# Kernel optimization log

Measured on AMD Instinct MI355X. Metric: run time of the kernel, lower is better.

## Reference

```python
import jax, jax.numpy as jnp
import numpy as np

K = 3          # hypergraph neighbors (hardcoded self.kn = 3)
H = 3          # attention heads (hardcoded num_heads=3)
QKD = 32       # qkv_dim
BN_EPS = 1e-5


def _pe(channels, num_frames):
    # Ter_Embed: sinusoidal over frame index, constant across joints -> (1,C,T,1)
    pos = jnp.arange(num_frames, dtype=jnp.float32)
    div = jnp.exp(jnp.arange(0, channels, 2, dtype=jnp.float32) * (-np.log(10000.0) / channels))
    ang = pos[:, None] * div[None, :]                      # (T, C/2)
    pe = jnp.zeros((num_frames, channels), jnp.float32)
    pe = pe.at[:, 0::2].set(jnp.sin(ang)).at[:, 1::2].set(jnp.cos(ang))
    return pe.T[None, :, :, None]                          # (1,C,T,1)


def _bn(x, g, b):
    # training-mode BatchNorm2d over (N,T,V) per channel
    mu = x.mean(axis=(0, 2, 3), keepdims=True)
    var = x.var(axis=(0, 2, 3), keepdims=True)
    return (x - mu) * jax.lax.rsqrt(var + BN_EPS) * g[None, :, None, None] + b[None, :, None, None]


def setup_inputs() -> dict:
    key = jax.random.key(0)
    ks = jax.random.split(key, 16)
    N, C, T, V = 8, 128, 64, 204
    s = 0.05
    inp = {
        'x': jax.random.normal(ks[0], (N, C, T, V), jnp.float32),
        # Transform.conv1: Conv1d(k, k*k, C, groups=k) -> weight (k*k, 1, C)
        'trans_w': jax.random.normal(ks[1], (K * K, C), jnp.float32) * s,
        'trans_b': jax.random.normal(ks[2], (K * K,), jnp.float32) * s,
        # VertexConv.convK1: Conv1d(k, 1, 1)
        'convk_w': jax.random.normal(ks[3], (K,), jnp.float32) * s,
        'convk_b': jax.random.normal(ks[4], (1,), jnp.float32) * s,
        # to_qkvs: Conv2d(C, 2*H*QKD, 1)
        'qkv_w': jax.random.normal(ks[5], (2 * H * QKD, C), jnp.float32) * s,
        'qkv_b': jax.random.normal(ks[6], (2 * H * QKD,), jnp.float32) * s,
        'alphas': jnp.ones((1, H, 1, 1), jnp.float32),
        'att1s': jnp.broadcast_to(jnp.eye(T, dtype=jnp.float32), (1, H, T, T)) + 0.0,
        # out_nets: Conv2d(H*C, C, (1,1)) + BN
        'out_w': jax.random.normal(ks[7], (C, H * C), jnp.float32) * s,
        'out_b': jax.random.normal(ks[8], (C,), jnp.float32) * s,
        'out_g': jnp.ones((C,), jnp.float32) + jax.random.normal(ks[9], (C,), jnp.float32) * 0.01,
        'out_beta': jax.random.normal(ks[10], (C,), jnp.float32) * 0.01,
        # ff_net: Conv2d(C, C, 1) + BN
        'ff_w': jax.random.normal(ks[11], (C, C), jnp.float32) * s,
        'ff_b': jax.random.normal(ks[12], (C,), jnp.float32) * s,
        'ff_g': jnp.ones((C,), jnp.float32) + jax.random.normal(ks[13], (C,), jnp.float32) * 0.01,
        'ff_beta': jax.random.normal(ks[14], (C,), jnp.float32) * 0.01,
    }
    return inp


def reference(x, trans_w, trans_b, convk_w, convk_b, qkv_w, qkv_b, alphas, att1s,
              out_w, out_b, out_g, out_beta, ff_w, ff_b, ff_g, ff_beta):
    N, C, T, V = x.shape
    orign = x
    # ---------- hypergraph_knn (ssa) ----------
    # cos_dis: F.normalize over last dim (V) then contract c,t -> (N,V,V)
    nrm = jnp.linalg.norm(x, axis=-1, keepdims=True)
    xn = x / jnp.maximum(nrm, 1e-12)
    dis = jnp.einsum('nctu,nctv->nuv', xn, xn)
    _, idx = jax.lax.top_k(dis, K)                                   # (N,V,K)
    # gather neighbor feats: feats[n,c,t,v,k] = x[n,c,t,idx[n,v,k]]
    feats = jnp.take_along_axis(x[:, :, :, None, :], idx[:, None, None, :, :], axis=4)  # (N,C,T,V,K)
    # Transform: grouped Conv1d over C, group g -> K outputs
    m = feats.mean(axis=2).transpose(0, 2, 3, 1)                     # (N,V,K,C)
    mult = jnp.einsum('nvgc,gpc->nvgp', m, trans_w.reshape(K, K, C)) + trans_b.reshape(K, K)
    mult = jax.nn.softmax(mult, axis=-1)                             # (N,V,K,K)
    transformed = jnp.einsum('nctvk,nvkp->nctvp', feats, mult)
    # convK1 pools K -> 1
    pooled = jnp.einsum('nctvk,k->nctv', transformed, convk_w) + convk_b[0]
    x = jax.nn.relu(pooled + orign)
    # ---------- TTA_Block_att ----------
    xs = x + _pe(C, T)
    qkv = jnp.einsum('oc,nctv->notv', qkv_w, xs) + qkv_b[None, :, None, None]
    qkv = qkv.reshape(N, 2 * H, QKD, T, V)
    q, k = qkv[:, :H], qkv[:, H:]
    att = jnp.tanh(jnp.einsum('nhctv,nhcqv->nhtq', q, k) / (QKD * V)) * alphas + att1s  # (N,H,T,T)
    xs2 = jnp.einsum('nctv,nstq->nscqv', x, att).reshape(N, H * C, T, V)
    out = jnp.einsum('os,nstv->notv', out_w, xs2) + out_b[None, :, None, None]
    out = _bn(out, out_g, out_beta)
    xs3 = jax.nn.leaky_relu(out + x, 0.1)                            # ress is identity (in==out)
    ff = jnp.einsum('oc,nctv->notv', ff_w, xs3) + ff_b[None, :, None, None]
    ff = _bn(ff, ff_g, ff_beta)
    return jax.nn.leaky_relu(ff + x, 0.1)
```

## Files before the change

### kernel.cpp

```cpp
#include <hip/hip_runtime.h>
#include <math.h>

#define N_ 8
#define C_ 128
#define T_ 64
#define V_ 204
#define H_ 3
#define QKD_ 32
#define O2_ 192
#define TV_ 13056
#define CT_ 8192
#define TT_ 4096
#define VV_ 41616
#define NCTV_ 13369344ull
#define DSPLIT_ 32
#define ZR_ 208
#define NBLK_ 1632

typedef __attribute__((ext_vector_type(8))) short short8v;
typedef __attribute__((ext_vector_type(4))) float f32x4;

__device__ inline unsigned short bf16rnd(float f) {
  union { float f; unsigned u; } x; x.f = f;
  return (unsigned short)((x.u + 0x7FFFu + ((x.u >> 16) & 1u)) >> 16);
}
__device__ inline float bf2f(unsigned short u) {
  union { unsigned u; float f; } x; x.u = ((unsigned)u) << 16;
  return x.f;
}

__global__ void k_wprep(const float* __restrict__ qw, const float* __restrict__ ow,
                        const float* __restrict__ fw, unsigned short* __restrict__ wb) {
  int g = blockIdx.x * 256 + threadIdx.x;
  if (g >= 704 * 16) return;
  int row = g >> 4, ch = g & 15;
  const float* src;
  if (row < 192) src = qw + row * 128;
  else if (row < 576) { int r = row - 192; src = ow + (r & 127) * 384 + (r >> 7) * 128; }
  else src = fw + (row - 576) * 128;
  f32x4 a = *(const f32x4*)(src + ch * 8);
  f32x4 b = *(const f32x4*)(src + ch * 8 + 4);
  unsigned short buf[8];
  buf[0] = bf16rnd(a.x); buf[1] = bf16rnd(a.y); buf[2] = bf16rnd(a.z); buf[3] = bf16rnd(a.w);
  buf[4] = bf16rnd(b.x); buf[5] = bf16rnd(b.y); buf[6] = bf16rnd(b.z); buf[7] = bf16rnd(b.w);
  *(uint4*)(wb + (size_t)row * 128 + ch * 8) = *(const uint4*)buf;
}

__global__ void k_qkvpe(const float* __restrict__ qw, const float* __restrict__ qb,
                        float* __restrict__ qpe) {
  __shared__ float pes[C_ * T_];
  int tid = threadIdx.x;
  for (int i = tid; i < C_ * T_; i += 256) {
    int t = i & 63, c = i >> 6;
    int j = c >> 1;
    float dv = expf((2.0f * j) * (-logf(10000.0f) / (float)C_));
    float ang = (float)t * dv;
    pes[i] = (c & 1) ? cosf(ang) : sinf(ang);
  }
  __syncthreads();
  int g = blockIdx.x * 256 + tid;
  int t = g & 63, m = g >> 6;
  float a = 0.f;
  for (int c = 0; c < C_; ++c) a += qw[m * C_ + c] * pes[c * T_ + t];
  qpe[g] = a + qb[m];
}

__global__ void k_scale(const float* __restrict__ x, float* __restrict__ s) {
  int gid = blockIdx.x * blockDim.x + threadIdx.x;
  int w = gid >> 6, lane = gid & 63;
  if (w >= N_ * CT_) return;
  const f32x4* row = (const f32x4*)(x + (size_t)w * V_);
  float a = 0.f;
  for (int v4 = lane; v4 < 51; v4 += 64) {
    f32x4 t = row[v4];
    a += t.x * t.x + t.y * t.y + t.z * t.z + t.w * t.w;
  }
#pragma unroll
  for (int off = 32; off >= 1; off >>= 1) a += __shfl_down(a, off, 64);
  if (lane == 0) {
    float d = fmaxf(sqrtf(a), 1e-12f);
    s[w] = 1.0f / (d * d);
  }
}

__global__ __launch_bounds__(256) void k_zprep(const float* __restrict__ x,
                                               const float* __restrict__ s,
                                               unsigned short* __restrict__ zhi,
                                               unsigned short* __restrict__ zlo,
                                               float* __restrict__ cm) {
  int kt = blockIdx.x, ut = blockIdx.y, n = blockIdx.z;
  int k0 = kt * 64, u0 = ut * 64;
  __shared__ float Ts[64][65];
  __shared__ float sq[64];
  int tid = threadIdx.x;
  int uu = tid & 63, kk = tid >> 6;
  int u = u0 + uu;
  bool uok = u < V_;
  const float* xb = x + (size_t)n * CT_ * V_;
#pragma unroll
  for (int it = 0; it < 16; ++it) {
    int kr = kk + it * 4;
    Ts[kr][uu] = uok ? xb[(size_t)(k0 + kr) * V_ + u] : 0.f;
  }
  if (tid < 64) sq[tid] = sqrtf(s[(size_t)n * CT_ + k0 + tid]);
  __syncthreads();
  if (tid < 64 && uok) {
    float a = 0.f;
    for (int t = 0; t < 64; ++t) a += Ts[t][tid];
    cm[((size_t)n * C_ + kt) * V_ + u] = a * (1.0f / 64.0f);
  }
#pragma unroll
  for (int it = 0; it < 4; ++it) {
    int sl = tid + it * 256;
    int u_l = sl & 63, oct = (sl >> 6) & 7, half = sl >> 9;
    int ug = u0 + u_l;
    if (ug >= ZR_) continue;
    unsigned short buf[8];
    if (ug < V_) {
#pragma unroll
      for (int j = 0; j < 8; ++j) {
        float z = Ts[oct * 8 + j][u_l] * sq[oct * 8 + j];
        unsigned short h = bf16rnd(z);
        buf[j] = half ? bf16rnd(z - bf2f(h)) : h;
      }
    } else {
#pragma unroll
      for (int j = 0; j < 8; ++j) buf[j] = 0;
    }
    unsigned short* dst = (half ? zlo : zhi) +
                          (((size_t)n * 1024 + kt * 8 + oct) * ZR_ + ug) * 8;
    *(uint4*)dst = *(const uint4*)buf;
  }
}

__global__ __launch_bounds__(256) void k_dism(const unsigned short* __restrict__ zhi,
                                              const unsigned short* __restrict__ zlo,
                                              float* __restrict__ pdis) {
  int q = blockIdx.x, sp = blockIdx.y, n = blockIdx.z;
  int bu = (q == 2) ? 1 : 0, bv = (q == 0) ? 0 : 1;
  int u0 = bu * 128, v0 = bv * 128;
  bool dg = (bu == bv);
  __shared__ unsigned short As[8 * 128 * 8];
  __shared__ unsigned short Bs[8 * 128 * 8];
  int tid = threadIdx.x, lane = tid & 63, wid = tid >> 6;
  int lr = lane & 15, lg = lane >> 4;
  f32x4 acc[2][8];
#pragma unroll
  for (int mi = 0; mi < 2; ++mi)
#pragma unroll
    for (int li = 0; li < 8; ++li) acc[mi][li] = (f32x4){0.f, 0.f, 0.f, 0.f};
  const int KCH = CT_ / DSPLIT_;
  int kbase = sp * KCH, kend = kbase + KCH;
  for (int kk = kbase; kk < kend; kk += 32) {
    int koct = kk >> 3;
    __syncthreads();
#pragma unroll
    for (int it = 0; it < 4; ++it) {
      int sl = tid + it * 256;
      int row = sl & 127, hs = sl >> 7;
      int slot = hs & 3, half = hs >> 2;
      const unsigned short* src = half ? zlo : zhi;
      size_t ob = ((size_t)n * 1024 + koct + slot) * ZR_;
      int ra = u0 + row; ra = ra > 207 ? 207 : ra;
      *(uint4*)&As[(hs * 128 + row) * 8] = *(const uint4*)(src + (ob + ra) * 8);
      if (!dg) {
        int rb = v0 + row; rb = rb > 207 ? 207 : rb;
        *(uint4*)&Bs[(hs * 128 + row) * 8] = *(const uint4*)(src + (ob + rb) * 8);
      }
    }
    __syncthreads();
    const unsigned short* Bp = dg ? As : Bs;
    short8v ah[2], al[2];
#pragma unroll
    for (int mi = 0; mi < 2; ++mi) {
      int r = wid * 32 + mi * 16 + lr;
      ah[mi] = *(const short8v*)&As[(lg * 128 + r) * 8];
      al[mi] = *(const short8v*)&As[((4 + lg) * 128 + r) * 8];
    }
#pragma unroll
    for (int li = 0; li < 8; ++li) {
      int rv = li * 16 + lr;
      short8v bh = *(const short8v*)&Bp[(lg * 128 + rv) * 8];
      short8v bl = *(const short8v*)&Bp[((4 + lg) * 128 + rv) * 8];
#pragma unroll
      for (int mi = 0; mi < 2; ++mi) {
        acc[mi][li] = __builtin_amdgcn_mfma_f32_16x16x32_bf16(ah[mi], bh, acc[mi][li], 0, 0, 0);
        acc[mi][li] = __builtin_amdgcn_mfma_f32_16x16x32_bf16(ah[mi], bl, acc[mi][li], 0, 0, 0);
        acc[mi][li] = __builtin_amdgcn_mfma_f32_16x16x32_bf16(al[mi], bh, acc[mi][li], 0, 0, 0);
      }
    }
  }
  float* pb = pdis + ((size_t)sp * N_ + n) * VV_;
#pragma unroll
  for (int mi = 0; mi < 2; ++mi) {
#pragma unroll
    for (int li = 0; li < 8; ++li) {
      int v = v0 + li * 16 + lr;
      if (v >= V_) continue;
#pragma unroll
      for (int rr = 0; rr < 4; ++rr) {
        int u = u0 + wid * 32 + mi * 16 + lg * 4 + rr;
        if (u >= V_) continue;
        float val = acc[mi][li][rr];
        pb[(size_t)u * V_ + v] = val;
        if (!dg) pb[(size_t)v * V_ + u] = val;
      }
    }
  }
}

__global__ void k_topk2(const float* __restrict__ pdis, int* __restrict__ idx) {
  int r = blockIdx.x;
  int n = r / V_, u = r - n * V_;
  int lane = threadIdx.x;
  float m0 = -INFINITY, m1 = -INFINITY, m2 = -INFINITY;
  int i0 = 0x7fffffff, i1 = 0x7fffffff, i2 = 0x7fffffff;
#pragma unroll
  for (int g = 0; g < 4; ++g) {
    int v = g * 64 + lane;
    if (v >= V_) break;
    float a = 0.f;
#pragma unroll
    for (int sp = 0; sp < DSPLIT_; ++sp)
      a += pdis[((size_t)sp * N_ + n) * VV_ + (size_t)u * V_ + v];
    if (a > m0 || (a == m0 && v < i0)) {
      m2 = m1; i2 = i1; m1 = m0; i1 = i0; m0 = a; i0 = v;
    } else if (a > m1 || (a == m1 && v < i1)) {
      m2 = m1; i2 = i1; m1 = a; i1 = v;
    } else if (a > m2 || (a == m2 && v < i2)) {
      m2 = a; i2 = v;
    }
  }
#pragma unroll
  for (int msk = 1; msk < 64; msk <<= 1) {
    float o0 = __shfl_xor(m0, msk, 64), o1 = __shfl_xor(m1, msk, 64),
          o2 = __shfl_xor(m2, msk, 64);
    int p0 = __shfl_xor(i0, msk, 64), p1 = __shfl_xor(i1, msk, 64),
        p2 = __shfl_xor(i2, msk, 64);
    float ov[3] = {o0, o1, o2};
    int op[3] = {p0, p1, p2};
#pragma unroll
    for (int e = 0; e < 3; ++e) {
      float a = ov[e]; int v = op[e];
      if (a > m0 || (a == m0 && v < i0)) {
        m2 = m1; i2 = i1; m1 = m0; i1 = i0; m0 = a; i0 = v;
      } else if (a > m1 || (a == m1 && v < i1)) {
        m2 = m1; i2 = i1; m1 = a; i1 = v;
      } else if (a > m2 || (a == m2 && v < i2)) {
        m2 = a; i2 = v;
      }
    }
  }
  if (lane == 0) {
    idx[r * 3 + 0] = i0; idx[r * 3 + 1] = i1; idx[r * 3 + 2] = i2;
  }
}

__global__ void k_w2(const float* __restrict__ cm, const int* __restrict__ idx,
                     const float* __restrict__ tw, const float* __restrict__ tb,
                     const float* __restrict__ ckw, float* __restrict__ w2) {
  int r = blockIdx.x;
  int n = r / V_;
  int lane = threadIdx.x;
  __shared__ float mv[3][C_];
  const int* ib = idx + r * 3;
  int j0 = ib[0], j1 = ib[1], j2 = ib[2];
  const float* cmn = cm + (size_t)n * C_ * V_;
  for (int c = lane; c < C_; c += 64) {
    mv[0][c] = cmn[c * V_ + j0];
    mv[1][c] = cmn[c * V_ + j1];
    mv[2][c] = cmn[c * V_ + j2];
  }
  __syncthreads();
  float p[9];
#pragma unroll
  for (int gp = 0; gp < 9; ++gp) p[gp] = 0.f;
  for (int c = lane; c < C_; c += 64) {
#pragma unroll
    for (int g = 0; g < 3; ++g) {
      float m = mv[g][c];
#pragma unroll
      for (int pp = 0; pp < 3; ++pp) p[g * 3 + pp] += m * tw[(g * 3 + pp) * C_ + c];
    }
  }
#pragma unroll
  for (int off = 32; off >= 1; off >>= 1) {
#pragma unroll
    for (int gp = 0; gp < 9; ++gp) p[gp] += __shfl_down(p[gp], off, 64);
  }
  if (lane == 0) {
    float c0 = ckw[0], c1 = ckw[1], c2 = ckw[2];
#pragma unroll
    for (int g = 0; g < 3; ++g) {
      float m0 = p[g * 3 + 0] + tb[g * 3 + 0];
      float m1 = p[g * 3 + 1] + tb[g * 3 + 1];
      float m2 = p[g * 3 + 2] + tb[g * 3 + 2];
      float mx = fmaxf(m0, fmaxf(m1, m2));
      float e0 = expf(m0 - mx), e1 = expf(m1 - mx), e2 = expf(m2 - mx);
      float inv = 1.0f / (e0 + e1 + e2);
      w2[r * 3 + g] = (e0 * c0 + e1 * c1 + e2 * c2) * inv;
    }
  }
}

__global__ __launch_bounds__(256) void k_x1p(const float* __restrict__ x,
                                             const int* __restrict__ idx,
                                             const float* __restrict__ w2,
                                             const float* __restrict__ ckb,
                                             unsigned short* __restrict__ x1pb) {
  int t = blockIdx.x, ct = blockIdx.y, n = blockIdx.z;
  int c0 = ct * 32;
  __shared__ float Ts[32][209];
  __shared__ int iw[V_ * 3];
  __shared__ float ww[V_ * 3];
  int tid = threadIdx.x;
  const float* xb = x + ((size_t)n * C_ + c0) * TV_ + t * V_;
  for (int i = tid; i < 32 * V_; i += 256) {
    int c = i / V_, v = i - c * V_;
    Ts[c][v] = xb[(size_t)c * TV_ + v];
  }
  for (int i = tid; i < V_ * 3; i += 256) {
    iw[i] = idx[(size_t)n * V_ * 3 + i];
    ww[i] = w2[(size_t)n * V_ * 3 + i];
  }
  __syncthreads();
  float cb = ckb[0];
  for (int i = tid; i < 32 * V_; i += 256) {
    int v = i >> 5, cl = i & 31;
    int b = v * 3;
    float pooled = Ts[cl][iw[b]] * ww[b] + Ts[cl][iw[b + 1]] * ww[b + 1] +
                   Ts[cl][iw[b + 2]] * ww[b + 2] + cb;
    float val = fmaxf(pooled + Ts[cl][v], 0.f);
    x1pb[((size_t)(n * V_ + v) * T_ + t) * C_ + c0 + cl] = bf16rnd(val);
  }
}

template <int MCH, int OBF, int STATS>
__global__ __launch_bounds__(256) void k_gmm2(const unsigned short* __restrict__ Wb,
                                              const unsigned short* __restrict__ Xp,
                                              const float* __restrict__ addv,
                                              void* __restrict__ Yv,
                                              float* __restrict__ part) {
  int l0 = blockIdx.x * 128, n = blockIdx.z;
  __shared__ unsigned short Xs[128 * 136];
  __shared__ unsigned short Ys[64 * 128];
  int tid = threadIdx.x, lane = tid & 63, wid = tid >> 6;
  int wm = wid >> 1, wl = wid & 1;
  int lr = lane & 15, lg = lane >> 4;
  const unsigned short* xb = Xp + ((size_t)n * TV_ + l0) * 128;
#pragma unroll
  for (int it = 0; it < 8; ++it) {
    int g = tid + it * 256;
    int row = g >> 4, ch = g & 15;
    *(uint4*)&Xs[row * 136 + ch * 8] = *(const uint4*)(xb + (size_t)row * 128 + ch * 8);
  }
  __syncthreads();
  for (int mc = 0; mc < MCH; ++mc) {
    short8v a[2][4];
#pragma unroll
    for (int mi = 0; mi < 2; ++mi) {
      int m = mc * 64 + wm * 32 + mi * 16 + lr;
#pragma unroll
      for (int ks = 0; ks < 4; ++ks)
        a[mi][ks] = *(const short8v*)(Wb + (size_t)m * 128 + ks * 32 + lg * 8);
    }
    f32x4 acc[2][4];
#pragma unroll
    for (int mi = 0; mi < 2; ++mi)
#pragma unroll
      for (int li = 0; li < 4; ++li) acc[mi][li] = (f32x4){0.f, 0.f, 0.f, 0.f};
#pragma unroll
    for (int ks = 0; ks < 4; ++ks) {
#pragma unroll
      for (int li = 0; li < 4; ++li) {
        short8v b = *(const short8v*)&Xs[(wl * 64 + li * 16 + lr) * 136 + ks * 32 + lg * 8];
#pragma unroll
        for (int mi = 0; mi < 2; ++mi)
          acc[mi][li] = __builtin_amdgcn_mfma_f32_16x16x32_bf16(a[mi][ks], b, acc[mi][li], 0, 0, 0);
      }
    }
    if (OBF) {
      __syncthreads();
#pragma unroll
      for (int mi = 0; mi < 2; ++mi)
#pragma unroll
        for (int li = 0; li < 4; ++li) {
          int lloc = wl * 64 + li * 16 + lr;
          int tt = (l0 + lloc) & 63;
#pragma unroll
          for (int r = 0; r < 4; ++r) {
            int mloc = wm * 32 + mi * 16 + lg * 4 + r;
            float val = acc[mi][li][r] + addv[(mc * 64 + mloc) * 64 + tt];
            Ys[mloc * 128 + lloc] = bf16rnd(val);
          }
        }
      __syncthreads();
      unsigned short* Yh = (unsigned short*)Yv;
#pragma unroll
      for (int it = 0; it < 4; ++it) {
        int g = tid + it * 256;
        int row = g >> 4, ch = g & 15;
        *(uint4*)(Yh + ((size_t)n * O2_ + mc * 64 + row) * TV_ + l0 + ch * 8) =
            *(const uint4*)&Ys[row * 128 + ch * 8];
      }
    } else {
      unsigned short* Yh = (unsigned short*)Yv;
      float st1[2][4] = {}, st2[2][4] = {};
#pragma unroll
      for (int mi = 0; mi < 2; ++mi)
#pragma unroll
        for (int li = 0; li < 4; ++li) {
          int lp = l0 + wl * 64 + li * 16 + lr;
          int m = mc * 64 + wm * 32 + mi * 16 + lg * 4;
          unsigned short b4[4];
#pragma unroll
          for (int r = 0; r < 4; ++r) {
            float val = acc[mi][li][r] + addv[m + r];
            if (STATS) { st1[mi][r] += val; st2[mi][r] += val * val; }
            b4[r] = bf16rnd(val);
          }
          *(uint2*)(Yh + ((size_t)n * TV_ + lp) * 128 + m) = *(const uint2*)b4;
        }
      if (STATS) {
        int blk2 = ((n * gridDim.x + blockIdx.x) * 2 + wl) * 256;
#pragma unroll
        for (int mi = 0; mi < 2; ++mi)
#pragma unroll
          for (int r = 0; r < 4; ++r) {
            float a1 = st1[mi][r], a2 = st2[mi][r];
            a1 += __shfl_xor(a1, 1, 64); a2 += __shfl_xor(a2, 1, 64);
            a1 += __shfl_xor(a1, 2, 64); a2 += __shfl_xor(a2, 2, 64);
            a1 += __shfl_xor(a1, 4, 64); a2 += __shfl_xor(a2, 4, 64);
            a1 += __shfl_xor(a1, 8, 64); a2 += __shfl_xor(a2, 8, 64);
            if (lr == 0) {
              int m = mc * 64 + wm * 32 + mi * 16 + lg * 4 + r;
              part[blk2 + m] = a1;
              part[blk2 + 128 + m] = a2;
            }
          }
      }
    }
  }
}

__global__ __launch_bounds__(256) void k_att(const unsigned short* __restrict__ qkv,
                                             float* __restrict__ attp) {
  int cp = blockIdx.x, h = blockIdx.y, n = blockIdx.z;
  __shared__ float Qs[102][68], Ks[102][68];
  int tid = threadIdx.x;
  int ty = tid >> 4, tx = tid & 15;
  float acc[4][4] = {};
  for (int cc = 0; cc < 2; ++cc) {
    int c = cp * 2 + cc;
    const unsigned short* qb = qkv + ((size_t)n * O2_ + h * QKD_ + c) * TV_;
    const unsigned short* kb = qkv + ((size_t)n * O2_ + H_ * QKD_ + h * QKD_ + c) * TV_;
    for (int vh = 0; vh < 2; ++vh) {
      for (int g = tid; g < 816; g += 256) {
        int v = g >> 3, t0 = (g & 7) * 8;
        uint4 qv = *(const uint4*)(qb + vh * 6528 + g * 8);
        uint4 kv = *(const uint4*)(kb + vh * 6528 + g * 8);
        const unsigned short* qs = (const unsigned short*)&qv;
        const unsigned short* ks2 = (const unsigned short*)&kv;
#pragma unroll
        for (int j = 0; j < 8; ++j) {
          Qs[v][t0 + j] = bf2f(qs[j]);
          Ks[v][t0 + j] = bf2f(ks2[j]);
        }
      }
      __syncthreads();
      for (int vv = 0; vv < 102; ++vv) {
        f32x4 qa = *(const f32x4*)&Qs[vv][ty * 4];
        f32x4 ka = *(const f32x4*)&Ks[vv][tx * 4];
#pragma unroll
        for (int i = 0; i < 4; ++i)
#pragma unroll
          for (int j = 0; j < 4; ++j) acc[i][j] += qa[i] * ka[j];
      }
      __syncthreads();
    }
  }
  float* ar = attp + (((size_t)cp * N_ + n) * H_ + h) * TT_;
#pragma unroll
  for (int i = 0; i < 4; ++i)
#pragma unroll
    for (int j = 0; j < 4; ++j)
      ar[(ty * 4 + i) * T_ + tx * 4 + j] = acc[i][j];
}

__global__ void k_attfin(const float* __restrict__ attp, const float* __restrict__ alphas,
                         const float* __restrict__ att1s, unsigned short* __restrict__ attT) {
  int i = blockIdx.x * blockDim.x + threadIdx.x;
  if (i >= N_ * H_ * TT_) return;
  int tt = i % TT_;
  int h = (i / TT_) % H_;
  int n = i / (H_ * TT_);
  float raw = 0.f;
#pragma unroll
  for (int cp = 0; cp < 16; ++cp)
    raw += attp[(((size_t)cp * N_ + n) * H_ + h) * TT_ + tt];
  int t = tt >> 6, q = tt & 63;
  float v = tanhf(raw * (1.0f / 6528.0f)) * alphas[h] + att1s[h * TT_ + tt];
  attT[(size_t)(n * 64 + q) * 192 + h * 64 + t] = bf16rnd(v);
}

__global__ __launch_bounds__(256) void k_fcomb(const unsigned short* __restrict__ x1pb,
                                               const unsigned short* __restrict__ w3b,
                                               const unsigned short* __restrict__ attT,
                                               const float* __restrict__ outb,
                                               unsigned short* __restrict__ preb,
                                               float* __restrict__ part) {
  int v = blockIdx.x, n = blockIdx.z;
  __shared__ unsigned short Yv[2][128 * 68];
  int tid = threadIdx.x, lane = tid & 63, wid = tid >> 6;
  int lr = lane & 15, lg = lane >> 4;
  const unsigned short* xb = x1pb + ((size_t)(n * V_ + v) * T_) * 128;
  short8v bx[4][4];
#pragma unroll
  for (int ks = 0; ks < 4; ++ks)
#pragma unroll
    for (int li = 0; li < 4; ++li)
      bx[ks][li] = *(const short8v*)(xb + (size_t)(li * 16 + lr) * 128 + ks * 32 + lg * 8);
  f32x4 acc2[4][2];
#pragma unroll
  for (int mq = 0; mq < 4; ++mq)
#pragma unroll
    for (int oi = 0; oi < 2; ++oi) acc2[mq][oi] = (f32x4){0.f, 0.f, 0.f, 0.f};
  const unsigned short* ab = attT + (size_t)n * 64 * 192;
  for (int h = 0; h < H_; ++h) {
    unsigned short* Yc = Yv[h & 1];
    short8v a1[2][4];
#pragma unroll
    for (int mi = 0; mi < 2; ++mi) {
      int m = wid * 32 + mi * 16 + lr;
#pragma unroll
      for (int ks = 0; ks < 4; ++ks)
        a1[mi][ks] = *(const short8v*)(w3b + ((size_t)(h * 128 + m)) * 128 + ks * 32 + lg * 8);
    }
    f32x4 acc1[2][4];
#pragma unroll
    for (int mi = 0; mi < 2; ++mi)
#pragma unroll
      for (int li = 0; li < 4; ++li) acc1[mi][li] = (f32x4){0.f, 0.f, 0.f, 0.f};
#pragma unroll
    for (int ks = 0; ks < 4; ++ks)
#pragma unroll
      for (int li = 0; li < 4; ++li)
#pragma unroll
        for (int mi = 0; mi < 2; ++mi)
          acc1[mi][li] = __builtin_amdgcn_mfma_f32_16x16x32_bf16(a1[mi][ks], bx[ks][li],
                                                                 acc1[mi][li], 0, 0, 0);
#pragma unroll
    for (int mi = 0; mi < 2; ++mi)
#pragma unroll
      for (int li = 0; li < 4; ++li) {
        int t = li * 16 + lr;
#pragma unroll
        for (int r = 0; r < 4; ++r) {
          int o = wid * 32 + mi * 16 + lg * 4 + r;
          Yc[o * 68 + t] = bf16rnd(acc1[mi][li][r]);
        }
      }
    __syncthreads();
#pragma unroll
    for (int ks2 = 0; ks2 < 2; ++ks2) {
      short8v bY[2];
#pragma unroll
      for (int oi = 0; oi < 2; ++oi)
        bY[oi] = *(const short8v*)&Yc[(wid * 32 + oi * 16 + lr) * 68 + ks2 * 32 + lg * 8];
#pragma unroll
      for (int mq = 0; mq < 4; ++mq) {
        short8v a2 = *(const short8v*)(ab + (size_t)(mq * 16 + lr) * 192 + h * 64 + ks2 * 32 + lg * 8);
#pragma unroll
        for (int oi = 0; oi < 2; ++oi)
          acc2[mq][oi] = __builtin_amdgcn_mfma_f32_16x16x32_bf16(a2, bY[oi], acc2[mq][oi], 0, 0, 0);
      }
    }
  }
  unsigned short* Ys2 = Yv[1];
  float s1[2] = {0.f, 0.f}, s2[2] = {0.f, 0.f};
#pragma unroll
  for (int mq = 0; mq < 4; ++mq)
#pragma unroll
    for (int oi = 0; oi < 2; ++oi) {
      int o = wid * 32 + oi * 16 + lr;
      float bo = outb[o];
#pragma unroll
      for (int r = 0; r < 4; ++r) {
        int q = mq * 16 + lg * 4 + r;
        float val = acc2[mq][oi][r] + bo;
        s1[oi] += val; s2[oi] += val * val;
        Ys2[q * 136 + o] = bf16rnd(val);
      }
    }
  int blk = (n * V_ + v) * 256;
#pragma unroll
  for (int oi = 0; oi < 2; ++oi) {
    float a1 = s1[oi], a2 = s2[oi];
    a1 += __shfl_xor(a1, 16, 64); a2 += __shfl_xor(a2, 16, 64);
    a1 += __shfl_xor(a1, 32, 64); a2 += __shfl_xor(a2, 32, 64);
    if ((lane & 48) == 0) {
      int o = wid * 32 + oi * 16 + lr;
      part[blk + o] = a1;
      part[blk + 128 + o] = a2;
    }
  }
  __syncthreads();
  unsigned short* ob2 = preb + ((size_t)(n * V_ + v) * T_) * 128;
#pragma unroll
  for (int it = 0; it < 4; ++it) {
    int g = tid + it * 256;
    int row = g >> 4, ch = g & 15;
    *(uint4*)(ob2 + (size_t)row * 128 + ch * 8) = *(const uint4*)&Ys2[row * 136 + ch * 8];
  }
}

__global__ void k_bnab(const float* __restrict__ part, const float* __restrict__ g,
                       const float* __restrict__ beta, float* __restrict__ ab) {
  int c = blockIdx.x;
  int tid = threadIdx.x;
  float s1 = 0.f, s2 = 0.f;
  for (int b = tid; b < NBLK_; b += 256) {
    s1 += part[b * 256 + c];
    s2 += part[b * 256 + 128 + c];
  }
  __shared__ float r1[256], r2[256];
  r1[tid] = s1; r2[tid] = s2;
  __syncthreads();
  for (int off = 128; off >= 1; off >>= 1) {
    if (tid < off) { r1[tid] += r1[tid + off]; r2[tid] += r2[tid + off]; }
    __syncthreads();
  }
  if (tid == 0) {
    const float cnt = (float)(N_ * TV_);
    float mu = r1[0] / cnt;
    float rstd = rsqrtf(r2[0] / cnt - mu * mu + 1e-5f);
    float a = rstd * g[c];
    ab[c] = a;
    ab[128 + c] = beta[c] - mu * a;
  }
}

__global__ void k_bnxt(const unsigned short* __restrict__ preb,
                       const unsigned short* __restrict__ x1pb,
                       const float* __restrict__ ab, unsigned short* __restrict__ xt) {
  __shared__ float sa[128], sb[128];
  int tid = threadIdx.x;
  if (tid < 128) { sa[tid] = ab[tid]; sb[tid] = ab[128 + tid]; }
  __syncthreads();
  const unsigned NU = (unsigned)(NCTV_ / 8);
  const uint4* p4 = (const uint4*)preb;
  const uint4* r4 = (const uint4*)x1pb;
  for (unsigned u = blockIdx.x * 256u + tid; u < NU; u += gridDim.x * 256u) {
    int c8 = (u & 15) * 8;
    uint4 pv = p4[u], rv = r4[u];
    const unsigned short* ps = (const unsigned short*)&pv;
    const unsigned short* rs = (const unsigned short*)&rv;
    unsigned short buf[8];
#pragma unroll
    for (int j = 0; j < 8; ++j) {
      float t = bf2f(ps[j]) * sa[c8 + j] + sb[c8 + j] + bf2f(rs[j]);
      buf[j] = bf16rnd(t > 0.f ? t : 0.1f * t);
    }
    *(uint4*)(xt + (size_t)u * 8) = *(const uint4*)buf;
  }
}

__global__ __launch_bounds__(256) void k_bnfinal(const unsigned short* __restrict__ preb,
                                                 const unsigned short* __restrict__ x1pb,
                                                 const float* __restrict__ ab,
                                                 float* __restrict__ dout) {
  int ct = blockIdx.x, t = blockIdx.y, n = blockIdx.z;
  int c0 = ct * 32;
  __shared__ float Tf[V_][33];
  __shared__ float sa[32], sb[32];
  int tid = threadIdx.x;
  if (tid < 32) { sa[tid] = ab[c0 + tid]; sb[tid] = ab[128 + c0 + tid]; }
  __syncthreads();
  for (int i = tid; i < V_ * 4; i += 256) {
    int v = i >> 2, ch = i & 3;
    size_t a = ((size_t)(n * V_ + v) * T_ + t) * 128 + c0 + ch * 8;
    uint4 pv = *(const uint4*)(preb + a);
    uint4 rv = *(const uint4*)(x1pb + a);
    const unsigned short* ps = (const unsigned short*)&pv;
    const unsigned short* rs = (const unsigned short*)&rv;
#pragma unroll
    for (int j = 0; j < 8; ++j) {
      int cl = ch * 8 + j;
      float val = bf2f(ps[j]) * sa[cl] + sb[cl] + bf2f(rs[j]);
      Tf[v][cl] = val > 0.f ? val : 0.1f * val;
    }
  }
  __syncthreads();
  for (int i = tid; i < 32 * V_; i += 256) {
    int cl = i / V_, v = i - cl * V_;
    dout[((size_t)(n * C_ + c0 + cl) * T_ + t) * V_ + v] = Tf[v][cl];
  }
}

extern "C" void kernel_launch(void* const* d_in, const int* in_sizes, int n_in,
                              void* d_out, int out_size, void* d_ws, size_t ws_size,
                              hipStream_t stream) {
  (void)in_sizes; (void)n_in; (void)out_size; (void)ws_size;
  const float* x        = (const float*)d_in[0];
  const float* trans_w  = (const float*)d_in[1];
  const float* trans_b  = (const float*)d_in[2];
  const float* convk_w  = (const float*)d_in[3];
  const float* convk_b  = (const float*)d_in[4];
  const float* qkv_w    = (const float*)d_in[5];
  const float* qkv_b    = (const float*)d_in[6];
  const float* alphas   = (const float*)d_in[7];
  const float* att1s    = (const float*)d_in[8];
  const float* out_w    = (const float*)d_in[9];
  const float* out_b    = (const float*)d_in[10];
  const float* out_g    = (const float*)d_in[11];
  const float* out_beta = (const float*)d_in[12];
  const float* ff_w     = (const float*)d_in[13];
  const float* ff_b     = (const float*)d_in[14];
  const float* ff_g     = (const float*)d_in[15];
  const float* ff_beta  = (const float*)d_in[16];

  float* ws = (float*)d_ws;
  size_t off = 0;
  float* gq = ws + off; off += (size_t)N_ * O2_ * TV_ / 2 + NCTV_ / 2;
  float* pdis = gq;
  unsigned short* qkvb = (unsigned short*)gq;
  unsigned short* preb = (unsigned short*)(gq + (size_t)N_ * O2_ * TV_ / 2);
  float* sbuf = ws + off; off += (size_t)N_ * CT_;
  int*   idx  = (int*)(ws + off); off += (size_t)N_ * V_ * 3 + 4;
  float* cm   = ws + off; off += (size_t)N_ * C_ * V_;
  float* w2   = ws + off; off += (size_t)N_ * V_ * 3 + 4;
  float* attp = ws + off; off += (size_t)16 * N_ * H_ * TT_;
  unsigned short* attT = (unsigned short*)(ws + off); off += (size_t)N_ * 64 * 192 / 2;
  float* part = ws + off; off += (size_t)NBLK_ * 256;
  float* ab   = ws + off; off += 512;
  float* qpe  = ws + off; off += (size_t)O2_ * T_;
  unsigned short* wb = (unsigned short*)(ws + off); off += 704 * 128 / 2;
  const size_t ZEL = (size_t)N_ * 1024 * ZR_ * 8;
  unsigned short* zhi = (unsigned short*)(ws + off);
  unsigned short* zlo = zhi + ZEL;
  off += ZEL;
  unsigned short* x1pb  = zhi;
  unsigned short* xs3pb = zlo;
  float* dout = (float*)d_out;

  k_wprep<<<44, 256, 0, stream>>>(qkv_w, out_w, ff_w, wb);
  k_qkvpe<<<48, 256, 0, stream>>>(qkv_w, qkv_b, qpe);
  k_scale<<<(N_ * CT_ * 64) / 256, 256, 0, stream>>>(x, sbuf);
  k_zprep<<<dim3(128, 4, N_), 256, 0, stream>>>(x, sbuf, zhi, zlo, cm);
  k_dism<<<dim3(3, DSPLIT_, N_), 256, 0, stream>>>(zhi, zlo, pdis);
  k_topk2<<<N_ * V_, 64, 0, stream>>>(pdis, idx);
  k_w2<<<N_ * V_, 64, 0, stream>>>(cm, idx, trans_w, trans_b, convk_w, w2);
  k_x1p<<<dim3(64, 4, N_), 256, 0, stream>>>(x, idx, w2, convk_b, x1pb);

  k_gmm2<3, 1, 0><<<dim3(102, 1, N_), 256, 0, stream>>>(wb, x1pb, qpe, qkvb, nullptr);
  k_att<<<dim3(16, H_, N_), 256, 0, stream>>>(qkvb, attp);
  k_attfin<<<384, 256, 0, stream>>>(attp, alphas, att1s, attT);

  k_fcomb<<<dim3(204, 1, N_), 256, 0, stream>>>(x1pb, wb + 192 * 128, attT, out_b, preb, part);

  k_bnab<<<128, 256, 0, stream>>>(part, out_g, out_beta, ab);
  k_bnxt<<<2048, 256, 0, stream>>>(preb, x1pb, ab, xs3pb);

  k_gmm2<2, 0, 1><<<dim3(102, 1, N_), 256, 0, stream>>>(wb + 576 * 128, xs3pb, ff_b, preb, part);
  k_bnab<<<128, 256, 0, stream>>>(part, ff_g, ff_beta, ab + 256);
  k_bnfinal<<<dim3(4, 64, N_), 256, 0, stream>>>(preb, x1pb, ab + 256, dout);
}
```

Measured before the change: 323.6 us.

## Repartition fcomb per-wave over time rows and use direct global-to-LDS loads

In the fused attention/out-projection kernel, each wave now owns 16 time rows and all 128 output channels, loading weights directly from global per MFMA. This replaces the previous output-channel split and shrinks the LDS buffer to a single Y tile. BN partial sums are written per wave, so the partial buffer and the k_bnab reduction count grow fourfold. Separately, the dismat kernel stages tiles through global_load_lds instead of register round-trips, which reduces VGPR traffic but changes the LDS write layout to linear slot order.

```diff
diff --git a/kernel.cpp b/kernel.cpp
--- a/kernel.cpp
+++ b/kernel.cpp
@@ -15,7 +15,6 @@
 #define NCTV_ 13369344ull
 #define DSPLIT_ 32
 #define ZR_ 208
-#define NBLK_ 1632
 
 typedef __attribute__((ext_vector_type(8))) short short8v;
 typedef __attribute__((ext_vector_type(4))) float f32x4;
@@ -27,6 +26,10 @@
 __device__ inline float bf2f(unsigned short u) {
   union { unsigned u; float f; } x; x.u = ((unsigned)u) << 16;
   return x.f;
+}
+__device__ inline void gload_lds16(const unsigned short* g, unsigned short* l) {
+  __builtin_amdgcn_global_load_lds((const __attribute__((address_space(1))) void*)g,
+                                   (__attribute__((address_space(3))) void*)l, 16, 0, 0);
 }
 
 __global__ void k_wprep(const float* __restrict__ qw, const float* __restrict__ ow,
@@ -162,10 +165,10 @@
       const unsigned short* src = half ? zlo : zhi;
       size_t ob = ((size_t)n * 1024 + koct + slot) * ZR_;
       int ra = u0 + row; ra = ra > 207 ? 207 : ra;
-      *(uint4*)&As[(hs * 128 + row) * 8] = *(const uint4*)(src + (ob + ra) * 8);
+      gload_lds16(src + (ob + ra) * 8, &As[sl * 8]);
       if (!dg) {
         int rb = v0 + row; rb = rb > 207 ? 207 : rb;
-        *(uint4*)&Bs[(hs * 128 + row) * 8] = *(const uint4*)(src + (ob + rb) * 8);
+        gload_lds16(src + (ob + rb) * 8, &Bs[sl * 8]);
       }
     }
     __syncthreads();
@@ -510,98 +513,76 @@
                                                unsigned short* __restrict__ preb,
                                                float* __restrict__ part) {
   int v = blockIdx.x, n = blockIdx.z;
-  __shared__ unsigned short Yv[2][128 * 68];
+  __shared__ unsigned short Yv[128 * 68];
   int tid = threadIdx.x, lane = tid & 63, wid = tid >> 6;
   int lr = lane & 15, lg = lane >> 4;
   const unsigned short* xb = x1pb + ((size_t)(n * V_ + v) * T_) * 128;
-  short8v bx[4][4];
+  short8v bx[4];
 #pragma unroll
   for (int ks = 0; ks < 4; ++ks)
-#pragma unroll
-    for (int li = 0; li < 4; ++li)
-      bx[ks][li] = *(const short8v*)(xb + (size_t)(li * 16 + lr) * 128 + ks * 32 + lg * 8);
-  f32x4 acc2[4][2];
-#pragma unroll
-  for (int mq = 0; mq < 4; ++mq)
-#pragma unroll
-    for (int oi = 0; oi < 2; ++oi) acc2[mq][oi] = (f32x4){0.f, 0.f, 0.f, 0.f};
+    bx[ks] = *(const short8v*)(xb + (size_t)(wid * 16 + lr) * 128 + ks * 32 + lg * 8);
+  f32x4 acc2[8];
+#pragma unroll
+  for (int oi = 0; oi < 8; ++oi) acc2[oi] = (f32x4){0.f, 0.f, 0.f, 0.f};
   const unsigned short* ab = attT + (size_t)n * 64 * 192;
+#pragma unroll
   for (int h = 0; h < H_; ++h) {
-    unsigned short* Yc = Yv[h & 1];
-    short8v a1[2][4];
-#pragma unroll
-    for (int mi = 0; mi < 2; ++mi) {
-      int m = wid * 32 + mi * 16 + lr;
-#pragma unroll
-      for (int ks = 0; ks < 4; ++ks)
-        a1[mi][ks] = *(const short8v*)(w3b + ((size_t)(h * 128 + m)) * 128 + ks * 32 + lg * 8);
-    }
-    f32x4 acc1[2][4];
-#pragma unroll
-    for (int mi = 0; mi < 2; ++mi)
-#pragma unroll
-      for (int li = 0; li < 4; ++li) acc1[mi][li] = (f32x4){0.f, 0.f, 0.f, 0.f};
-#pragma unroll
-    for (int ks = 0; ks < 4; ++ks)
-#pragma unroll
-      for (int li = 0; li < 4; ++li)
-#pragma unroll
-        for (int mi = 0; mi < 2; ++mi)
-          acc1[mi][li] = __builtin_amdgcn_mfma_f32_16x16x32_bf16(a1[mi][ks], bx[ks][li],
-                                                                 acc1[mi][li], 0, 0, 0);
-#pragma unroll
-    for (int mi = 0; mi < 2; ++mi)
-#pragma unroll
-      for (int li = 0; li < 4; ++li) {
-        int t = li * 16 + lr;
-#pragma unroll
-        for (int r = 0; r < 4; ++r) {
-          int o = wid * 32 + mi * 16 + lg * 4 + r;
-          Yc[o * 68 + t] = bf16rnd(acc1[mi][li][r]);
-        }
-      }
+    f32x4 acc1[8];
+#pragma unroll
+    for (int mi = 0; mi < 8; ++mi) {
+      acc1[mi] = (f32x4){0.f, 0.f, 0.f, 0.f};
+      const unsigned short* wr = w3b + ((size_t)(h * 128 + mi * 16 + lr)) * 128;
+#pragma unroll
+      for (int ks = 0; ks < 4; ++ks) {
+        short8v a1 = *(const short8v*)(wr + ks * 32 + lg * 8);
+        acc1[mi] = __builtin_amdgcn_mfma_f32_16x16x32_bf16(a1, bx[ks], acc1[mi], 0, 0, 0);
+      }
+    }
     __syncthreads();
+    int t = wid * 16 + lr;
+#pragma unroll
+    for (int mi = 0; mi < 8; ++mi)
+#pragma unroll
+      for (int r = 0; r < 4; ++r) {
+        int o = mi * 16 + lg * 4 + r;
+        Yv[o * 68 + t] = bf16rnd(acc1[mi][r]);
+      }
+    __syncthreads();
 #pragma unroll
     for (int ks2 = 0; ks2 < 2; ++ks2) {
-      short8v bY[2];
-#pragma unroll
-      for (int oi = 0; oi < 2; ++oi)
-        bY[oi] = *(const short8v*)&Yc[(wid * 32 + oi * 16 + lr) * 68 + ks2 * 32 + lg * 8];
-#pragma unroll
-      for (int mq = 0; mq < 4; ++mq) {
-        short8v a2 = *(const short8v*)(ab + (size_t)(mq * 16 + lr) * 192 + h * 64 + ks2 * 32 + lg * 8);
-#pragma unroll
-        for (int oi = 0; oi < 2; ++oi)
-          acc2[mq][oi] = __builtin_amdgcn_mfma_f32_16x16x32_bf16(a2, bY[oi], acc2[mq][oi], 0, 0, 0);
-      }
-    }
-  }
-  unsigned short* Ys2 = Yv[1];
-  float s1[2] = {0.f, 0.f}, s2[2] = {0.f, 0.f};
-#pragma unroll
-  for (int mq = 0; mq < 4; ++mq)
-#pragma unroll
-    for (int oi = 0; oi < 2; ++oi) {
-      int o = wid * 32 + oi * 16 + lr;
-      float bo = outb[o];
-#pragma unroll
-      for (int r = 0; r < 4; ++r) {
-        int q = mq * 16 + lg * 4 + r;
-        float val = acc2[mq][oi][r] + bo;
-        s1[oi] += val; s2[oi] += val * val;
-        Ys2[q * 136 + o] = bf16rnd(val);
-      }
-    }
-  int blk = (n * V_ + v) * 256;
-#pragma unroll
-  for (int oi = 0; oi < 2; ++oi) {
-    float a1 = s1[oi], a2 = s2[oi];
-    a1 += __shfl_xor(a1, 16, 64); a2 += __shfl_xor(a2, 16, 64);
-    a1 += __shfl_xor(a1, 32, 64); a2 += __shfl_xor(a2, 32, 64);
-    if ((lane & 48) == 0) {
-      int o = wid * 32 + oi * 16 + lr;
-      part[blk + o] = a1;
-      part[blk + 128 + o] = a2;
+      short8v a2 = *(const short8v*)(ab + (size_t)(wid * 16 + lr) * 192 + h * 64 + ks2 * 32 + lg * 8);
+#pragma unroll
+      for (int oi = 0; oi < 8; ++oi) {
+        short8v bY = *(const short8v*)&Yv[(oi * 16 + lr) * 68 + ks2 * 32 + lg * 8];
+        acc2[oi] = __builtin_amdgcn_mfma_f32_16x16x32_bf16(a2, bY, acc2[oi], 0, 0, 0);
+      }
+    }
+  }
+  __syncthreads();
+  float s1o[8], s2o[8];
+#pragma unroll
+  for (int oi = 0; oi < 8; ++oi) {
+    int o = oi * 16 + lr;
+    float bo = outb[o];
+    float s1 = 0.f, s2 = 0.f;
+#pragma unroll
+    for (int r = 0; r < 4; ++r) {
+      int qq = wid * 16 + lg * 4 + r;
+      float val = acc2[oi][r] + bo;
+      s1 += val; s2 += val * val;
+      Yv[qq * 136 + o] = bf16rnd(val);
+    }
+    s1o[oi] = s1; s2o[oi] = s2;
+  }
+  int blk = ((n * V_ + v) * 4 + wid) * 256;
+#pragma unroll
+  for (int oi = 0; oi < 8; ++oi) {
+    float a1 = s1o[oi], a2v = s2o[oi];
+    a1 += __shfl_xor(a1, 16, 64); a2v += __shfl_xor(a2v, 16, 64);
+    a1 += __shfl_xor(a1, 32, 64); a2v += __shfl_xor(a2v, 32, 64);
+    if (lg == 0) {
+      part[blk + oi * 16 + lr] = a1;
+      part[blk + 128 + oi * 16 + lr] = a2v;
     }
   }
   __syncthreads();
@@ -610,16 +591,17 @@
   for (int it = 0; it < 4; ++it) {
     int g = tid + it * 256;
     int row = g >> 4, ch = g & 15;
-    *(uint4*)(ob2 + (size_t)row * 128 + ch * 8) = *(const uint4*)&Ys2[row * 136 + ch * 8];
-  }
-}
-
-__global__ void k_bnab(const float* __restrict__ part, const float* __restrict__ g,
-                       const float* __restrict__ beta, float* __restrict__ ab) {
+    *(uint4*)(ob2 + (size_t)row * 128 + ch * 8) = *(const uint4*)&Yv[row * 136 + ch * 8];
+  }
+}
+
+__global__ void k_bnab(const float* __restrict__ part, int count,
+                       const float* __restrict__ g, const float* __restrict__ beta,
+                       float* __restrict__ ab) {
   int c = blockIdx.x;
   int tid = threadIdx.x;
   float s1 = 0.f, s2 = 0.f;
-  for (int b = tid; b < NBLK_; b += 256) {
+  for (int b = tid; b < count; b += 256) {
     s1 += part[b * 256 + c];
     s2 += part[b * 256 + 128 + c];
   }
@@ -731,7 +713,7 @@
   float* w2   = ws + off; off += (size_t)N_ * V_ * 3 + 4;
   float* attp = ws + off; off += (size_t)16 * N_ * H_ * TT_;
   unsigned short* attT = (unsigned short*)(ws + off); off += (size_t)N_ * 64 * 192 / 2;
-  float* part = ws + off; off += (size_t)NBLK_ * 256;
+  float* part = ws + off; off += (size_t)6528 * 256;
   float* ab   = ws + off; off += 512;
   float* qpe  = ws + off; off += (size_t)O2_ * T_;
   unsigned short* wb = (unsigned short*)(ws + off); off += 704 * 128 / 2;
@@ -758,10 +740,10 @@
 
   k_fcomb<<<dim3(204, 1, N_), 256, 0, stream>>>(x1pb, wb + 192 * 128, attT, out_b, preb, part);
 
-  k_bnab<<<128, 256, 0, stream>>>(part, out_g, out_beta, ab);
+  k_bnab<<<128, 256, 0, stream>>>(part, 6528, out_g, out_beta, ab);
   k_bnxt<<<2048, 256, 0, stream>>>(preb, x1pb, ab, xs3pb);
 
   k_gmm2<2, 0, 1><<<dim3(102, 1, N_), 256, 0, stream>>>(wb + 576 * 128, xs3pb, ff_b, preb, part);
-  k_bnab<<<128, 256, 0, stream>>>(part, ff_g, ff_beta, ab + 256);
+  k_bnab<<<128, 256, 0, stream>>>(part, 1632, ff_g, ff_beta, ab + 256);
   k_bnfinal<<<dim3(4, 64, N_), 256, 0, stream>>>(preb, x1pb, ab + 256, dout);
 }
```

Measured after the change: 367.0 us. 1.13x slower.

## Move attention scores to MFMA with position-major qkv layout and async LDS loads

Applied to the files above, without the earlier changes.

The QKV GEMM now writes its output position-major (row per (v,t), 192 channels) instead of channel-major through an LDS transpose. The scalar-FMA attention-score kernel is replaced by one that reads q/k fragments straight from global memory into bf16 MFMA ops, splitting V across waves and reducing in LDS. The distance kernel's tile loads switch to direct global-to-LDS loads, and an extra barrier is added in the fused combine kernel. The aim is to cut the scalar FLOP cost of the attention scores and the LDS staging overhead, at the risk of strided 16-byte global reads in the new attention kernel.

```diff
diff --git a/kernel.cpp b/kernel.cpp
--- a/kernel.cpp
+++ b/kernel.cpp
@@ -28,6 +28,10 @@
   union { unsigned u; float f; } x; x.u = ((unsigned)u) << 16;
   return x.f;
 }
+__device__ inline void gload_lds16(const unsigned short* g, unsigned short* l) {
+  __builtin_amdgcn_global_load_lds((const __attribute__((address_space(1))) void*)g,
+                                   (__attribute__((address_space(3))) void*)l, 16, 0, 0);
+}
 
 __global__ void k_wprep(const float* __restrict__ qw, const float* __restrict__ ow,
                         const float* __restrict__ fw, unsigned short* __restrict__ wb) {
@@ -162,10 +166,10 @@
       const unsigned short* src = half ? zlo : zhi;
       size_t ob = ((size_t)n * 1024 + koct + slot) * ZR_;
       int ra = u0 + row; ra = ra > 207 ? 207 : ra;
-      *(uint4*)&As[(hs * 128 + row) * 8] = *(const uint4*)(src + (ob + ra) * 8);
+      gload_lds16(src + (ob + ra) * 8, &As[sl * 8]);
       if (!dg) {
         int rb = v0 + row; rb = rb > 207 ? 207 : rb;
-        *(uint4*)&Bs[(hs * 128 + row) * 8] = *(const uint4*)(src + (ob + rb) * 8);
+        gload_lds16(src + (ob + rb) * 8, &Bs[sl * 8]);
       }
     }
     __syncthreads();
@@ -335,15 +339,15 @@
   }
 }
 
-template <int MCH, int OBF, int STATS>
+template <int MCH, int PEB, int STATS>
 __global__ __launch_bounds__(256) void k_gmm2(const unsigned short* __restrict__ Wb,
                                               const unsigned short* __restrict__ Xp,
                                               const float* __restrict__ addv,
-                                              void* __restrict__ Yv,
+                                              unsigned short* __restrict__ Yh,
                                               float* __restrict__ part) {
+  const int MS = MCH * 64;
   int l0 = blockIdx.x * 128, n = blockIdx.z;
   __shared__ unsigned short Xs[128 * 136];
-  __shared__ unsigned short Ys[64 * 128];
   int tid = threadIdx.x, lane = tid & 63, wid = tid >> 6;
   int wm = wid >> 1, wl = wid & 1;
   int lr = lane & 15, lg = lane >> 4;
@@ -379,112 +383,98 @@
           acc[mi][li] = __builtin_amdgcn_mfma_f32_16x16x32_bf16(a[mi][ks], b, acc[mi][li], 0, 0, 0);
       }
     }
-    if (OBF) {
-      __syncthreads();
+    float st1[2][4] = {}, st2[2][4] = {};
+#pragma unroll
+    for (int mi = 0; mi < 2; ++mi)
+#pragma unroll
+      for (int li = 0; li < 4; ++li) {
+        int lp = l0 + wl * 64 + li * 16 + lr;
+        int m = mc * 64 + wm * 32 + mi * 16 + lg * 4;
+        unsigned short b4[4];
+#pragma unroll
+        for (int r = 0; r < 4; ++r) {
+          float val = acc[mi][li][r] +
+                      (PEB ? addv[(m + r) * 64 + (lp & 63)] : addv[m + r]);
+          if (STATS) { st1[mi][r] += val; st2[mi][r] += val * val; }
+          b4[r] = bf16rnd(val);
+        }
+        *(uint2*)(Yh + ((size_t)n * TV_ + lp) * MS + m) = *(const uint2*)b4;
+      }
+    if (STATS) {
+      int blk2 = ((n * gridDim.x + blockIdx.x) * 2 + wl) * 256;
 #pragma unroll
       for (int mi = 0; mi < 2; ++mi)
 #pragma unroll
-        for (int li = 0; li < 4; ++li) {
-          int lloc = wl * 64 + li * 16 + lr;
-          int tt = (l0 + lloc) & 63;
-#pragma unroll
-          for (int r = 0; r < 4; ++r) {
-            int mloc = wm * 32 + mi * 16 + lg * 4 + r;
-            float val = acc[mi][li][r] + addv[(mc * 64 + mloc) * 64 + tt];
-            Ys[mloc * 128 + lloc] = bf16rnd(val);
+        for (int r = 0; r < 4; ++r) {
+          float a1 = st1[mi][r], a2 = st2[mi][r];
+          a1 += __shfl_xor(a1, 1, 64); a2 += __shfl_xor(a2, 1, 64);
+          a1 += __shfl_xor(a1, 2, 64); a2 += __shfl_xor(a2, 2, 64);
+          a1 += __shfl_xor(a1, 4, 64); a2 += __shfl_xor(a2, 4, 64);
+          a1 += __shfl_xor(a1, 8, 64); a2 += __shfl_xor(a2, 8, 64);
+          if (lr == 0) {
+            int m = mc * 64 + wm * 32 + mi * 16 + lg * 4 + r;
+            part[blk2 + m] = a1;
+            part[blk2 + 128 + m] = a2;
           }
         }
-      __syncthreads();
-      unsigned short* Yh = (unsigned short*)Yv;
-#pragma unroll
-      for (int it = 0; it < 4; ++it) {
-        int g = tid + it * 256;
-        int row = g >> 4, ch = g & 15;
-        *(uint4*)(Yh + ((size_t)n * O2_ + mc * 64 + row) * TV_ + l0 + ch * 8) =
-            *(const uint4*)&Ys[row * 128 + ch * 8];
-      }
-    } else {
-      unsigned short* Yh = (unsigned short*)Yv;
-      float st1[2][4] = {}, st2[2][4] = {};
-#pragma unroll
-      for (int mi = 0; mi < 2; ++mi)
-#pragma unroll
-        for (int li = 0; li < 4; ++li) {
-          int lp = l0 + wl * 64 + li * 16 + lr;
-          int m = mc * 64 + wm * 32 + mi * 16 + lg * 4;
-          unsigned short b4[4];
-#pragma unroll
-          for (int r = 0; r < 4; ++r) {
-            float val = acc[mi][li][r] + addv[m + r];
-            if (STATS) { st1[mi][r] += val; st2[mi][r] += val * val; }
-            b4[r] = bf16rnd(val);
-          }
-          *(uint2*)(Yh + ((size_t)n * TV_ + lp) * 128 + m) = *(const uint2*)b4;
-        }
-      if (STATS) {
-        int blk2 = ((n * gridDim.x + blockIdx.x) * 2 + wl) * 256;
-#pragma unroll
-        for (int mi = 0; mi < 2; ++mi)
-#pragma unroll
-          for (int r = 0; r < 4; ++r) {
-            float a1 = st1[mi][r], a2 = st2[mi][r];
-            a1 += __shfl_xor(a1, 1, 64); a2 += __shfl_xor(a2, 1, 64);
-            a1 += __shfl_xor(a1, 2, 64); a2 += __shfl_xor(a2, 2, 64);
-            a1 += __shfl_xor(a1, 4, 64); a2 += __shfl_xor(a2, 4, 64);
-            a1 += __shfl_xor(a1, 8, 64); a2 += __shfl_xor(a2, 8, 64);
-            if (lr == 0) {
-              int m = mc * 64 + wm * 32 + mi * 16 + lg * 4 + r;
-              part[blk2 + m] = a1;
-              part[blk2 + 128 + m] = a2;
-            }
-          }
-      }
-    }
-  }
-}
-
-__global__ __launch_bounds__(256) void k_att(const unsigned short* __restrict__ qkv,
-                                             float* __restrict__ attp) {
-  int cp = blockIdx.x, h = blockIdx.y, n = blockIdx.z;
-  __shared__ float Qs[102][68], Ks[102][68];
-  int tid = threadIdx.x;
-  int ty = tid >> 4, tx = tid & 15;
-  float acc[4][4] = {};
-  for (int cc = 0; cc < 2; ++cc) {
-    int c = cp * 2 + cc;
-    const unsigned short* qb = qkv + ((size_t)n * O2_ + h * QKD_ + c) * TV_;
-    const unsigned short* kb = qkv + ((size_t)n * O2_ + H_ * QKD_ + h * QKD_ + c) * TV_;
-    for (int vh = 0; vh < 2; ++vh) {
-      for (int g = tid; g < 816; g += 256) {
-        int v = g >> 3, t0 = (g & 7) * 8;
-        uint4 qv = *(const uint4*)(qb + vh * 6528 + g * 8);
-        uint4 kv = *(const uint4*)(kb + vh * 6528 + g * 8);
-        const unsigned short* qs = (const unsigned short*)&qv;
-        const unsigned short* ks2 = (const unsigned short*)&kv;
-#pragma unroll
-        for (int j = 0; j < 8; ++j) {
-          Qs[v][t0 + j] = bf2f(qs[j]);
-          Ks[v][t0 + j] = bf2f(ks2[j]);
-        }
-      }
-      __syncthreads();
-      for (int vv = 0; vv < 102; ++vv) {
-        f32x4 qa = *(const f32x4*)&Qs[vv][ty * 4];
-        f32x4 ka = *(const f32x4*)&Ks[vv][tx * 4];
-#pragma unroll
-        for (int i = 0; i < 4; ++i)
-#pragma unroll
-          for (int j = 0; j < 4; ++j) acc[i][j] += qa[i] * ka[j];
-      }
-      __syncthreads();
-    }
-  }
-  float* ar = attp + (((size_t)cp * N_ + n) * H_ + h) * TT_;
-#pragma unroll
-  for (int i = 0; i < 4; ++i)
-#pragma unroll
-    for (int j = 0; j < 4; ++j)
-      ar[(ty * 4 + i) * T_ + tx * 4 + j] = acc[i][j];
+    }
+  }
+}
+
+__global__ __launch_bounds__(256) void k_attm(const unsigned short* __restrict__ qkv,
+                                              float* __restrict__ attp) {
+  int vs = blockIdx.x, h = blockIdx.y, n = blockIdx.z;
+  __shared__ float buf[64 * 68];
+  int tid = threadIdx.x, lane = tid & 63, wid = tid >> 6;
+  int lr = lane & 15, lg = lane >> 4;
+  f32x4 acc[4][4];
+#pragma unroll
+  for (int ti = 0; ti < 4; ++ti)
+#pragma unroll
+    for (int qi = 0; qi < 4; ++qi) acc[ti][qi] = (f32x4){0.f, 0.f, 0.f, 0.f};
+  int vend = (vs + 1) * 13; if (vend > V_) vend = V_;
+  for (int v = vs * 13 + wid; v < vend; v += 4) {
+    const unsigned short* rb = qkv + ((size_t)n * TV_ + v * 64) * 192;
+    short8v a[4], b[4];
+#pragma unroll
+    for (int ti = 0; ti < 4; ++ti)
+      a[ti] = *(const short8v*)(rb + (size_t)(ti * 16 + lr) * 192 + h * 32 + lg * 8);
+#pragma unroll
+    for (int qi = 0; qi < 4; ++qi)
+      b[qi] = *(const short8v*)(rb + (size_t)(qi * 16 + lr) * 192 + 96 + h * 32 + lg * 8);
+#pragma unroll
+    for (int ti = 0; ti < 4; ++ti)
+#pragma unroll
+      for (int qi = 0; qi < 4; ++qi)
+        acc[ti][qi] = __builtin_amdgcn_mfma_f32_16x16x32_bf16(a[ti], b[qi], acc[ti][qi], 0, 0, 0);
+  }
+  if (wid == 0) {
+#pragma unroll
+    for (int ti = 0; ti < 4; ++ti)
+#pragma unroll
+      for (int qi = 0; qi < 4; ++qi)
+#pragma unroll
+        for (int r = 0; r < 4; ++r)
+          buf[(ti * 16 + lg * 4 + r) * 68 + qi * 16 + lr] = acc[ti][qi][r];
+  }
+  __syncthreads();
+  for (int w = 1; w < 4; ++w) {
+    if (wid == w) {
+#pragma unroll
+      for (int ti = 0; ti < 4; ++ti)
+#pragma unroll
+        for (int qi = 0; qi < 4; ++qi)
+#pragma unroll
+          for (int r = 0; r < 4; ++r)
+            buf[(ti * 16 + lg * 4 + r) * 68 + qi * 16 + lr] += acc[ti][qi][r];
+    }
+    __syncthreads();
+  }
+  float* ar = attp + (((size_t)vs * N_ + n) * H_ + h) * TT_;
+  int t = tid >> 2, q0 = (tid & 3) * 16;
+#pragma unroll
+  for (int j = 0; j < 4; ++j)
+    *(f32x4*)(ar + t * 64 + q0 + j * 4) = *(const f32x4*)&buf[t * 68 + q0 + j * 4];
 }
 
 __global__ void k_attfin(const float* __restrict__ attp, const float* __restrict__ alphas,
@@ -575,6 +565,7 @@
           acc2[mq][oi] = __builtin_amdgcn_mfma_f32_16x16x32_bf16(a2, bY[oi], acc2[mq][oi], 0, 0, 0);
       }
     }
+    __syncthreads();
   }
   unsigned short* Ys2 = Yv[1];
   float s1[2] = {0.f, 0.f}, s2[2] = {0.f, 0.f};
@@ -595,13 +586,13 @@
   int blk = (n * V_ + v) * 256;
 #pragma unroll
   for (int oi = 0; oi < 2; ++oi) {
-    float a1 = s1[oi], a2 = s2[oi];
-    a1 += __shfl_xor(a1, 16, 64); a2 += __shfl_xor(a2, 16, 64);
-    a1 += __shfl_xor(a1, 32, 64); a2 += __shfl_xor(a2, 32, 64);
+    float a1 = s1[oi], a2v = s2[oi];
+    a1 += __shfl_xor(a1, 16, 64); a2v += __shfl_xor(a2v, 16, 64);
+    a1 += __shfl_xor(a1, 32, 64); a2v += __shfl_xor(a2v, 32, 64);
     if ((lane & 48) == 0) {
       int o = wid * 32 + oi * 16 + lr;
       part[blk + o] = a1;
-      part[blk + 128 + o] = a2;
+      part[blk + 128 + o] = a2v;
     }
   }
   __syncthreads();
@@ -614,12 +605,13 @@
   }
 }
 
-__global__ void k_bnab(const float* __restrict__ part, const float* __restrict__ g,
-                       const float* __restrict__ beta, float* __restrict__ ab) {
+__global__ void k_bnab(const float* __restrict__ part, int count,
+                       const float* __restrict__ g, const float* __restrict__ beta,
+                       float* __restrict__ ab) {
   int c = blockIdx.x;
   int tid = threadIdx.x;
   float s1 = 0.f, s2 = 0.f;
-  for (int b = tid; b < NBLK_; b += 256) {
+  for (int b = tid; b < count; b += 256) {
     s1 += part[b * 256 + c];
     s2 += part[b * 256 + 128 + c];
   }
@@ -753,15 +745,15 @@
   k_x1p<<<dim3(64, 4, N_), 256, 0, stream>>>(x, idx, w2, convk_b, x1pb);
 
   k_gmm2<3, 1, 0><<<dim3(102, 1, N_), 256, 0, stream>>>(wb, x1pb, qpe, qkvb, nullptr);
-  k_att<<<dim3(16, H_, N_), 256, 0, stream>>>(qkvb, attp);
+  k_attm<<<dim3(16, H_, N_), 256, 0, stream>>>(qkvb, attp);
   k_attfin<<<384, 256, 0, stream>>>(attp, alphas, att1s, attT);
 
   k_fcomb<<<dim3(204, 1, N_), 256, 0, stream>>>(x1pb, wb + 192 * 128, attT, out_b, preb, part);
 
-  k_bnab<<<128, 256, 0, stream>>>(part, out_g, out_beta, ab);
+  k_bnab<<<128, 256, 0, stream>>>(part, NBLK_, out_g, out_beta, ab);
   k_bnxt<<<2048, 256, 0, stream>>>(preb, x1pb, ab, xs3pb);
 
   k_gmm2<2, 0, 1><<<dim3(102, 1, N_), 256, 0, stream>>>(wb + 576 * 128, xs3pb, ff_b, preb, part);
-  k_bnab<<<128, 256, 0, stream>>>(part, ff_g, ff_beta, ab + 256);
+  k_bnab<<<128, 256, 0, stream>>>(part, NBLK_, ff_g, ff_beta, ab + 256);
   k_bnfinal<<<dim3(4, 64, N_), 256, 0, stream>>>(preb, x1pb, ab + 256, dout);
 }
```

Result: faster. 315.5 us (-2.5%).
